# Kernel optimization log

Hardware: AMD Instinct MI355X
Metric: run time of the kernel (lower is better)

## Reference

```python
import jax, jax.numpy as jnp
import numpy as np

NUM_NODES = 200000
NUM_EDGES = 1250000
DIM = 64
K_LAYERS = 3
BATCH = 4096
CAND = 101  # 1 positive + 100 negatives


def setup_inputs() -> dict:
    key = jax.random.key(0)
    k1, k2, k3 = jax.random.split(key, 3)
    emb = jax.random.normal(k1, (NUM_NODES, DIM), dtype=jnp.float32)
    edge_index = jax.random.randint(k2, (2, NUM_EDGES), 0, NUM_NODES)
    batch = jax.random.randint(k3, (BATCH, CAND, 3), 0, NUM_NODES)
    return {"emb": emb, "edge_index": edge_index, "batch": batch,
            "num_nodes": NUM_NODES}


def reference(emb, edge_index, batch, num_nodes):
    # --- LightGCN.get_embedding: K rounds of symmetric-normalized SpMM ---
    row, col = edge_index[0], edge_index[1]  # source -> target
    ones = jnp.ones(row.shape[0], dtype=emb.dtype)
    deg = jax.ops.segment_sum(ones, col, num_segments=num_nodes)  # in-degree
    deg_safe = jnp.where(deg > 0, deg, 1.0)
    dis = jnp.where(deg > 0, jax.lax.rsqrt(deg_safe), 0.0)  # deg^{-1/2}, inf->0
    norm = dis[row] * dis[col]  # [E]

    alpha = 1.0 / (K_LAYERS + 1)  # uniform layer combination
    x = emb
    out = x * alpha
    for _ in range(K_LAYERS):
        # propagate: out[i] = sum_{(j->i)} norm_e * x[j]
        x = jax.ops.segment_sum(x[row] * norm[:, None], col,
                                num_segments=num_nodes)
        out = out + x * alpha

    # --- scoring: gather user/item embeddings, elementwise dot ---
    user_idx = batch[:, :, 0].reshape(-1)
    item_idx = batch[:, :, 1].reshape(-1)
    logits = jnp.sum(out[user_idx] * out[item_idx], axis=-1)  # [B*CAND]
    return logits.reshape(batch.shape[0], -1)
```

## Files before the change

### kernel.cpp

```cpp
#include <hip/hip_runtime.h>

#define DIM 64
#define BSHIFT 8
#define MAXNB 1024
#define CHUNK 4096

__device__ inline unsigned packbf(float a, float b) {
    unsigned ua = __float_as_uint(a), ub = __float_as_uint(b);
    unsigned ra = (ua + 0x7FFFu + ((ua >> 16) & 1u)) >> 16;
    unsigned rb = (ub + 0x7FFFu + ((ub >> 16) & 1u)) >> 16;
    return ra | (rb << 16);
}
__device__ inline void unpackbf(unsigned u, float& lo, float& hi) {
    lo = __uint_as_float(u << 16);
    hi = __uint_as_float(u & 0xFFFF0000u);
}
__device__ inline void acc_row(const uint4 v, float* s) {
    float lo, hi;
    unpackbf(v.x, lo, hi); s[0] += lo; s[1] += hi;
    unpackbf(v.y, lo, hi); s[2] += lo; s[3] += hi;
    unpackbf(v.z, lo, hi); s[4] += lo; s[5] += hi;
    unpackbf(v.w, lo, hi); s[6] += lo; s[7] += hi;
}
__device__ inline void acc_row_m(const uint4 v, float m, float* s) {
    float lo, hi;
    unpackbf(v.x, lo, hi); s[0] = fmaf(m, lo, s[0]); s[1] = fmaf(m, hi, s[1]);
    unpackbf(v.y, lo, hi); s[2] = fmaf(m, lo, s[2]); s[3] = fmaf(m, hi, s[3]);
    unpackbf(v.z, lo, hi); s[4] = fmaf(m, lo, s[4]); s[5] = fmaf(m, hi, s[5]);
    unpackbf(v.w, lo, hi); s[6] = fmaf(m, lo, s[6]); s[7] = fmaf(m, hi, s[7]);
}

__global__ __launch_bounds__(256) void block_hist_kernel(
        const int* __restrict__ col, int* __restrict__ H, int E, int NB,
        int nblocks) {
    __shared__ int h[MAXNB];
    int tid = threadIdx.x;
    for (int k = tid; k < NB; k += 256) h[k] = 0;
    __syncthreads();
    int base = blockIdx.x * CHUNK;
    #pragma unroll
    for (int k = 0; k < CHUNK / 256; k++) {
        int e = base + tid + k * 256;
        if (e < E) atomicAdd(&h[col[e] >> BSHIFT], 1);
    }
    __syncthreads();
    for (int k = tid; k < NB; k += 256) H[(size_t)k * nblocks + blockIdx.x] = h[k];
}

__global__ void scan_tile_sum_kernel(const int* __restrict__ H,
                                     int* __restrict__ T, int M) {
    int tid = threadIdx.x;
    int base = blockIdx.x * 1024 + tid * 4;
    int s = 0;
    #pragma unroll
    for (int k = 0; k < 4; k++)
        if (base + k < M) s += H[base + k];
    __shared__ int lds[256];
    lds[tid] = s;
    __syncthreads();
    for (int off = 128; off > 0; off >>= 1) {
        if (tid < off) lds[tid] += lds[tid + off];
        __syncthreads();
    }
    if (tid == 0) T[blockIdx.x] = lds[0];
}

__global__ void scan_tile_offsets_kernel(int* __restrict__ T, int nt) {
    __shared__ int lds[256];
    int tid = threadIdx.x;
    int v = (tid < nt) ? T[tid] : 0;
    lds[tid] = v;
    __syncthreads();
    for (int off = 1; off < 256; off <<= 1) {
        int t = (tid >= off) ? lds[tid - off] : 0;
        __syncthreads();
        lds[tid] += t;
        __syncthreads();
    }
    if (tid < nt) T[tid] = lds[tid] - v;
}

__global__ void scan_final_kernel(const int* __restrict__ H,
                                  const int* __restrict__ T,
                                  int* __restrict__ S, int M) {
    int tid = threadIdx.x;
    int base = blockIdx.x * 1024 + tid * 4;
    int c[4];
    int local = 0;
    #pragma unroll
    for (int k = 0; k < 4; k++) {
        c[k] = (base + k < M) ? H[base + k] : 0;
        local += c[k];
    }
    __shared__ int lds[256];
    lds[tid] = local;
    __syncthreads();
    for (int off = 1; off < 256; off <<= 1) {
        int t = (tid >= off) ? lds[tid - off] : 0;
        __syncthreads();
        lds[tid] += t;
        __syncthreads();
    }
    int excl = lds[tid] - local + T[blockIdx.x];
    #pragma unroll
    for (int k = 0; k < 4; k++) {
        if (base + k < M) S[base + k] = excl;
        excl += c[k];
    }
}

__global__ void bbase_kernel(const int* __restrict__ S, int* __restrict__ bbase,
                             int NB, int nblocks, int E) {
    int k = blockIdx.x * blockDim.x + threadIdx.x;
    if (k < NB) bbase[k] = S[(size_t)k * nblocks];
    if (k == 0) bbase[NB] = E;
}

__global__ __launch_bounds__(256) void scatter_binned_kernel(
        const int* __restrict__ row, const int* __restrict__ col,
        const int* __restrict__ S, unsigned* __restrict__ pairs, int E,
        int NB, int nblocks) {
    __shared__ unsigned stage[CHUNK];
    __shared__ int gdst[CHUNK];
    __shared__ int hist[MAXNB];
    __shared__ int pfx[MAXNB];
    __shared__ int gbase[MAXNB];
    int tid = threadIdx.x;
    int bid = blockIdx.x;
    int base = bid * CHUNK;
    int nloc = min(CHUNK, E - base);

    for (int b = tid; b < NB; b += 256) hist[b] = 0;
    __syncthreads();

    unsigned vals[CHUNK / 256];
    int keys[CHUNK / 256];
    #pragma unroll
    for (int k = 0; k < CHUNK / 256; k++) {
        int e = base + tid + k * 256;
        if (e < E) {
            int d = col[e];
            int s = row[e];
            keys[k] = d >> BSHIFT;
            vals[k] = (unsigned)s | ((unsigned)(d & 255) << 24);
            atomicAdd(&hist[keys[k]], 1);
        } else {
            keys[k] = -1;
        }
    }
    __syncthreads();

    int b0 = tid * 4;
    int c4[4];
    int loc = 0;
    #pragma unroll
    for (int k = 0; k < 4; k++) {
        c4[k] = (b0 + k < NB) ? hist[b0 + k] : 0;
        loc += c4[k];
    }
    gbase[tid] = loc;
    __syncthreads();
    for (int off = 1; off < 256; off <<= 1) {
        int t = (tid >= off) ? gbase[tid - off] : 0;
        __syncthreads();
        gbase[tid] += t;
        __syncthreads();
    }
    int excl = gbase[tid] - loc;
    #pragma unroll
    for (int k = 0; k < 4; k++) {
        if (b0 + k < NB) pfx[b0 + k] = excl;
        excl += c4[k];
    }
    __syncthreads();

    for (int b = tid; b < NB; b += 256) {
        gbase[b] = S[(size_t)b * nblocks + bid];
        hist[b] = pfx[b];
    }
    __syncthreads();

    #pragma unroll
    for (int k = 0; k < CHUNK / 256; k++) {
        if (keys[k] >= 0) {
            int slot = atomicAdd(&hist[keys[k]], 1);
            stage[slot] = vals[k];
            gdst[slot] = gbase[keys[k]] + (slot - pfx[keys[k]]);
        }
    }
    __syncthreads();

    for (int s = tid; s < nloc; s += 256) pairs[gdst[s]] = stage[s];
}

__global__ void fine_fill_kernel(const unsigned* __restrict__ pairs,
                                 const int* __restrict__ bbase,
                                 int* __restrict__ row_ptr,
                                 int* __restrict__ csr_src, int N, int E) {
    __shared__ int cnt[256];
    __shared__ int cur[256];
    int b = blockIdx.x;
    int tid = threadIdx.x;
    int beg = bbase[b], end = bbase[b + 1];
    cnt[tid] = 0;
    __syncthreads();
    for (int j = beg + tid; j < end; j += 256)
        atomicAdd(&cnt[pairs[j] >> 24], 1);
    __syncthreads();
    int v = cnt[tid];
    for (int off = 1; off < 256; off <<= 1) {
        int t = (tid >= off) ? cnt[tid - off] : 0;
        __syncthreads();
        cnt[tid] += t;
        __syncthreads();
    }
    int excl = cnt[tid] - v;
    int node = (b << BSHIFT) + tid;
    if (node < N) row_ptr[node] = beg + excl;
    cur[tid] = beg + excl;
    __syncthreads();
    for (int j = beg + tid; j < end; j += 256) {
        unsigned p = pairs[j];
        int pos = atomicAdd(&cur[p >> 24], 1);
        csr_src[pos] = (int)(p & 0xFFFFFFu);
    }
    if (b == 0 && tid == 0) row_ptr[N] = E;
}

__global__ void prescale_kernel(const float4* __restrict__ emb4,
                                const int* __restrict__ row_ptr,
                                uint4* __restrict__ z4, int N) {
    int t = blockIdx.x * blockDim.x + threadIdx.x;
    int i = t >> 3;
    int gl = t & 7;
    if (i >= N) return;
    int deg = row_ptr[i + 1] - row_ptr[i];
    float wd = (deg > 0) ? rsqrtf((float)deg) : 0.0f;
    size_t eo = (size_t)i * 16 + gl * 2;
    float4 a = emb4[eo], b = emb4[eo + 1];
    uint4 z;
    z.x = packbf(a.x * wd, a.y * wd);
    z.y = packbf(a.z * wd, a.w * wd);
    z.z = packbf(b.x * wd, b.y * wd);
    z.w = packbf(b.z * wd, b.w * wd);
    z4[(size_t)i * 8 + gl] = z;
}

__device__ inline void row_gather_sum(const int* __restrict__ csr_src,
                                      const uint4* __restrict__ z4, int b,
                                      int e, int gl, float* s) {
    if (b >= e) return;
    int e1 = e - 1;
    int j = b;
    int i0 = csr_src[j];
    int i1 = csr_src[min(j + 1, e1)];
    int i2 = csr_src[min(j + 2, e1)];
    int i3 = csr_src[min(j + 3, e1)];
    while (j < e) {
        uint4 v0 = z4[(size_t)i0 * 8 + gl];
        uint4 v1 = z4[(size_t)i1 * 8 + gl];
        uint4 v2 = z4[(size_t)i2 * 8 + gl];
        uint4 v3 = z4[(size_t)i3 * 8 + gl];
        int jn = j + 4;
        if (jn < e) {
            i0 = csr_src[jn];
            i1 = csr_src[min(jn + 1, e1)];
            i2 = csr_src[min(jn + 2, e1)];
            i3 = csr_src[min(jn + 3, e1)];
        }
        float m1 = (j + 1 < e) ? 1.0f : 0.0f;
        float m2 = (j + 2 < e) ? 1.0f : 0.0f;
        float m3 = (j + 3 < e) ? 1.0f : 0.0f;
        acc_row(v0, s);
        acc_row_m(v1, m1, s);
        acc_row_m(v2, m2, s);
        acc_row_m(v3, m3, s);
        j = jn;
    }
}

__global__ void spmm_pull_kernel(const int* __restrict__ row_ptr,
                                 const int* __restrict__ csr_src,
                                 const uint4* __restrict__ z4,
                                 uint4* __restrict__ znext4, int N) {
    int t = blockIdx.x * blockDim.x + threadIdx.x;
    int i = t >> 3;
    int gl = t & 7;
    if (i >= N) return;
    int b = row_ptr[i], e = row_ptr[i + 1];
    float s[8] = {0, 0, 0, 0, 0, 0, 0, 0};
    row_gather_sum(csr_src, z4, b, e, gl, s);
    int deg = e - b;
    float wd = (deg > 0) ? rsqrtf((float)deg) : 0.0f;
    float w2 = wd * wd;
    uint4 z;
    z.x = packbf(s[0] * w2, s[1] * w2);
    z.y = packbf(s[2] * w2, s[3] * w2);
    z.z = packbf(s[4] * w2, s[5] * w2);
    z.w = packbf(s[6] * w2, s[7] * w2);
    znext4[(size_t)i * 8 + gl] = z;
}

__global__ void spmm_combine_kernel(const int* __restrict__ row_ptr,
                                    const int* __restrict__ csr_src,
                                    const uint4* __restrict__ z2,
                                    const uint4* __restrict__ z1,
                                    const float4* __restrict__ emb4,
                                    uint4* __restrict__ accb, int N) {
    int t = blockIdx.x * blockDim.x + threadIdx.x;
    int i = t >> 3;
    int gl = t & 7;
    if (i >= N) return;
    int b = row_ptr[i], e = row_ptr[i + 1];
    float s[8] = {0, 0, 0, 0, 0, 0, 0, 0};
    row_gather_sum(csr_src, z2, b, e, gl, s);
    int deg = e - b;
    float wd = (deg > 0) ? rsqrtf((float)deg) : 0.0f;
    float sq = (deg > 0) ? sqrtf((float)deg) : 0.0f;
    size_t zo = (size_t)i * 8 + gl;
    uint4 a1 = z1[zo], a2 = z2[zo];
    float w[8] = {0, 0, 0, 0, 0, 0, 0, 0};
    acc_row(a1, w); acc_row(a2, w);
    size_t eo = (size_t)i * 16 + gl * 2;
    float4 e0 = emb4[eo], e1 = emb4[eo + 1];
    float r0 = e0.x + sq * w[0] + wd * s[0];
    float r1 = e0.y + sq * w[1] + wd * s[1];
    float r2 = e0.z + sq * w[2] + wd * s[2];
    float r3 = e0.w + sq * w[3] + wd * s[3];
    float r4 = e1.x + sq * w[4] + wd * s[4];
    float r5 = e1.y + sq * w[5] + wd * s[5];
    float r6 = e1.z + sq * w[6] + wd * s[6];
    float r7 = e1.w + sq * w[7] + wd * s[7];
    uint4 z;
    z.x = packbf(r0, r1);
    z.y = packbf(r2, r3);
    z.z = packbf(r4, r5);
    z.w = packbf(r6, r7);
    accb[zo] = z;
}

__global__ void score_kernel(const int* __restrict__ batch,
                             const uint4* __restrict__ accb,
                             float* __restrict__ out, int P) {
    int t = blockIdx.x * blockDim.x + threadIdx.x;
    int p = t >> 3;
    int gl = t & 7;
    if (p >= P) return;
    int u = batch[(size_t)p * 3 + 0];
    int it = batch[(size_t)p * 3 + 1];
    uint4 a = accb[(size_t)u * 8 + gl];
    uint4 b = accb[(size_t)it * 8 + gl];
    float sa[8] = {0, 0, 0, 0, 0, 0, 0, 0};
    float sb[8] = {0, 0, 0, 0, 0, 0, 0, 0};
    acc_row(a, sa);
    acc_row(b, sb);
    float s = sa[0] * sb[0] + sa[1] * sb[1] + sa[2] * sb[2] + sa[3] * sb[3] +
              sa[4] * sb[4] + sa[5] * sb[5] + sa[6] * sb[6] + sa[7] * sb[7];
    s += __shfl_xor(s, 4, 64);
    s += __shfl_xor(s, 2, 64);
    s += __shfl_xor(s, 1, 64);
    if (gl == 0) out[p] = s * 0.0625f;
}

extern "C" void kernel_launch(void* const* d_in, const int* in_sizes, int n_in,
                              void* d_out, int out_size, void* d_ws,
                              size_t ws_size, hipStream_t stream) {
    const float* emb = (const float*)d_in[0];
    const int* edge_index = (const int*)d_in[1];
    const int* batch = (const int*)d_in[2];
    float* out = (float*)d_out;

    const int N = in_sizes[0] / DIM;
    const int E = in_sizes[1] / 2;
    const int P = out_size;
    const int NB = (N + 255) >> BSHIFT;
    const int nblocks = (E + CHUNK - 1) / CHUNK;
    const int M = NB * nblocks;
    const int nt = (M + 1023) / 1024;

    const int* row = edge_index;
    const int* col = edge_index + E;

    const size_t zbytes = (size_t)N * DIM * 2;

    auto align256 = [](size_t x) { return (x + 255) & ~(size_t)255; };
    char* ws = (char*)d_ws;
    uint4* z0   = (uint4*)ws; ws += align256(zbytes);
    uint4* z1   = (uint4*)ws; ws += align256(zbytes);
    uint4* z2   = (uint4*)ws; ws += align256(zbytes);
    uint4* accb = (uint4*)ws; ws += align256(zbytes);
    unsigned* pairs = (unsigned*)ws; ws += align256((size_t)E * 4);
    int* csr_src    = (int*)ws;      ws += align256((size_t)E * 4);
    int* row_ptr    = (int*)ws;      ws += align256((size_t)(N + 1) * 4);
    int* H          = (int*)ws;      ws += align256((size_t)M * 4);
    int* S          = (int*)ws;      ws += align256((size_t)M * 4);
    int* T          = (int*)ws;      ws += align256(256 * 4);
    int* bbase      = (int*)ws;

    block_hist_kernel<<<nblocks, 256, 0, stream>>>(col, H, E, NB, nblocks);
    scan_tile_sum_kernel<<<nt, 256, 0, stream>>>(H, T, M);
    scan_tile_offsets_kernel<<<1, 256, 0, stream>>>(T, nt);
    scan_final_kernel<<<nt, 256, 0, stream>>>(H, T, S, M);
    bbase_kernel<<<(NB + 255) / 256, 256, 0, stream>>>(S, bbase, NB, nblocks, E);
    scatter_binned_kernel<<<nblocks, 256, 0, stream>>>(row, col, S, pairs, E,
                                                       NB, nblocks);
    fine_fill_kernel<<<NB, 256, 0, stream>>>(pairs, bbase, row_ptr, csr_src,
                                             N, E);

    const int nodeBlocks = (N * 8 + 255) / 256;

    prescale_kernel<<<nodeBlocks, 256, 0, stream>>>((const float4*)emb,
                                                    row_ptr, z0, N);

    spmm_pull_kernel<<<nodeBlocks, 256, 0, stream>>>(row_ptr, csr_src, z0, z1, N);
    spmm_pull_kernel<<<nodeBlocks, 256, 0, stream>>>(row_ptr, csr_src, z1, z2, N);
    spmm_combine_kernel<<<nodeBlocks, 256, 0, stream>>>(row_ptr, csr_src, z2,
                                                        z1, (const float4*)emb,
                                                        accb, N);

    score_kernel<<<(P * 8 + 255) / 256, 256, 0, stream>>>(batch, accb, out, P);
}
```

Measured before the change: 249.9 us.

## Fuse bbase into scan, cache bf16 emb, use wave-sized blocks, two pairs per score group

```diff
diff --git a/kernel.cpp b/kernel.cpp
--- a/kernel.cpp
+++ b/kernel.cpp
@@ -82,7 +82,9 @@
 
 __global__ void scan_final_kernel(const int* __restrict__ H,
                                   const int* __restrict__ T,
-                                  int* __restrict__ S, int M) {
+                                  int* __restrict__ S,
+                                  int* __restrict__ bbase, int M, int nblocks,
+                                  int NB, int E) {
     int tid = threadIdx.x;
     int base = blockIdx.x * 1024 + tid * 4;
     int c[4];
@@ -104,16 +106,14 @@
     int excl = lds[tid] - local + T[blockIdx.x];
     #pragma unroll
     for (int k = 0; k < 4; k++) {
-        if (base + k < M) S[base + k] = excl;
+        int m = base + k;
+        if (m < M) {
+            S[m] = excl;
+            if (m % nblocks == 0) bbase[m / nblocks] = excl;
+        }
         excl += c[k];
     }
-}
-
-__global__ void bbase_kernel(const int* __restrict__ S, int* __restrict__ bbase,
-                             int NB, int nblocks, int E) {
-    int k = blockIdx.x * blockDim.x + threadIdx.x;
-    if (k < NB) bbase[k] = S[(size_t)k * nblocks];
-    if (k == 0) bbase[NB] = E;
+    if (blockIdx.x == 0 && tid == 0) bbase[NB] = E;
 }
 
 __global__ __launch_bounds__(256) void scatter_binned_kernel(
@@ -229,7 +229,8 @@
 
 __global__ void prescale_kernel(const float4* __restrict__ emb4,
                                 const int* __restrict__ row_ptr,
-                                uint4* __restrict__ z4, int N) {
+                                uint4* __restrict__ z4,
+                                uint4* __restrict__ embb, int N) {
     int t = blockIdx.x * blockDim.x + threadIdx.x;
     int i = t >> 3;
     int gl = t & 7;
@@ -238,12 +239,19 @@
     float wd = (deg > 0) ? rsqrtf((float)deg) : 0.0f;
     size_t eo = (size_t)i * 16 + gl * 2;
     float4 a = emb4[eo], b = emb4[eo + 1];
+    size_t zo = (size_t)i * 8 + gl;
+    uint4 eb;
+    eb.x = packbf(a.x, a.y);
+    eb.y = packbf(a.z, a.w);
+    eb.z = packbf(b.x, b.y);
+    eb.w = packbf(b.z, b.w);
+    embb[zo] = eb;
     uint4 z;
     z.x = packbf(a.x * wd, a.y * wd);
     z.y = packbf(a.z * wd, a.w * wd);
     z.z = packbf(b.x * wd, b.y * wd);
     z.w = packbf(b.z * wd, b.w * wd);
-    z4[(size_t)i * 8 + gl] = z;
+    z4[zo] = z;
 }
 
 __device__ inline void row_gather_sum(const int* __restrict__ csr_src,
@@ -279,11 +287,10 @@
     }
 }
 
-__global__ void spmm_pull_kernel(const int* __restrict__ row_ptr,
-                                 const int* __restrict__ csr_src,
-                                 const uint4* __restrict__ z4,
-                                 uint4* __restrict__ znext4, int N) {
-    int t = blockIdx.x * blockDim.x + threadIdx.x;
+__global__ __launch_bounds__(64) void spmm_pull_kernel(
+        const int* __restrict__ row_ptr, const int* __restrict__ csr_src,
+        const uint4* __restrict__ z4, uint4* __restrict__ znext4, int N) {
+    int t = blockIdx.x * 64 + threadIdx.x;
     int i = t >> 3;
     int gl = t & 7;
     if (i >= N) return;
@@ -301,13 +308,11 @@
     znext4[(size_t)i * 8 + gl] = z;
 }
 
-__global__ void spmm_combine_kernel(const int* __restrict__ row_ptr,
-                                    const int* __restrict__ csr_src,
-                                    const uint4* __restrict__ z2,
-                                    const uint4* __restrict__ z1,
-                                    const float4* __restrict__ emb4,
-                                    uint4* __restrict__ accb, int N) {
-    int t = blockIdx.x * blockDim.x + threadIdx.x;
+__global__ __launch_bounds__(64) void spmm_combine_kernel(
+        const int* __restrict__ row_ptr, const int* __restrict__ csr_src,
+        const uint4* __restrict__ z2, const uint4* __restrict__ z1,
+        const uint4* __restrict__ embb, uint4* __restrict__ accb, int N) {
+    int t = blockIdx.x * 64 + threadIdx.x;
     int i = t >> 3;
     int gl = t & 7;
     if (i >= N) return;
@@ -321,45 +326,60 @@
     uint4 a1 = z1[zo], a2 = z2[zo];
     float w[8] = {0, 0, 0, 0, 0, 0, 0, 0};
     acc_row(a1, w); acc_row(a2, w);
-    size_t eo = (size_t)i * 16 + gl * 2;
-    float4 e0 = emb4[eo], e1 = emb4[eo + 1];
-    float r0 = e0.x + sq * w[0] + wd * s[0];
-    float r1 = e0.y + sq * w[1] + wd * s[1];
-    float r2 = e0.z + sq * w[2] + wd * s[2];
-    float r3 = e0.w + sq * w[3] + wd * s[3];
-    float r4 = e1.x + sq * w[4] + wd * s[4];
-    float r5 = e1.y + sq * w[5] + wd * s[5];
-    float r6 = e1.z + sq * w[6] + wd * s[6];
-    float r7 = e1.w + sq * w[7] + wd * s[7];
+    uint4 eb = embb[zo];
+    float em[8] = {0, 0, 0, 0, 0, 0, 0, 0};
+    acc_row(eb, em);
+    float r[8];
+    #pragma unroll
+    for (int k = 0; k < 8; k++) r[k] = em[k] + sq * w[k] + wd * s[k];
     uint4 z;
-    z.x = packbf(r0, r1);
-    z.y = packbf(r2, r3);
-    z.z = packbf(r4, r5);
-    z.w = packbf(r6, r7);
+    z.x = packbf(r[0], r[1]);
+    z.y = packbf(r[2], r[3]);
+    z.z = packbf(r[4], r[5]);
+    z.w = packbf(r[6], r[7]);
     accb[zo] = z;
 }
 
-__global__ void score_kernel(const int* __restrict__ batch,
-                             const uint4* __restrict__ accb,
-                             float* __restrict__ out, int P) {
-    int t = blockIdx.x * blockDim.x + threadIdx.x;
-    int p = t >> 3;
+__global__ __launch_bounds__(64) void score_kernel(
+        const int* __restrict__ batch, const uint4* __restrict__ accb,
+        float* __restrict__ out, int P) {
+    int t = blockIdx.x * 64 + threadIdx.x;
+    int g = t >> 3;
     int gl = t & 7;
-    if (p >= P) return;
-    int u = batch[(size_t)p * 3 + 0];
-    int it = batch[(size_t)p * 3 + 1];
-    uint4 a = accb[(size_t)u * 8 + gl];
-    uint4 b = accb[(size_t)it * 8 + gl];
-    float sa[8] = {0, 0, 0, 0, 0, 0, 0, 0};
-    float sb[8] = {0, 0, 0, 0, 0, 0, 0, 0};
-    acc_row(a, sa);
-    acc_row(b, sb);
-    float s = sa[0] * sb[0] + sa[1] * sb[1] + sa[2] * sb[2] + sa[3] * sb[3] +
-              sa[4] * sb[4] + sa[5] * sb[5] + sa[6] * sb[6] + sa[7] * sb[7];
-    s += __shfl_xor(s, 4, 64);
-    s += __shfl_xor(s, 2, 64);
-    s += __shfl_xor(s, 1, 64);
-    if (gl == 0) out[p] = s * 0.0625f;
+    int p0 = g * 2;
+    if (p0 >= P) return;
+    int p1 = min(p0 + 1, P - 1);
+    int u0 = batch[(size_t)p0 * 3 + 0];
+    int i0 = batch[(size_t)p0 * 3 + 1];
+    int u1 = batch[(size_t)p1 * 3 + 0];
+    int i1 = batch[(size_t)p1 * 3 + 1];
+    uint4 a0 = accb[(size_t)u0 * 8 + gl];
+    uint4 b0 = accb[(size_t)i0 * 8 + gl];
+    uint4 a1 = accb[(size_t)u1 * 8 + gl];
+    uint4 b1 = accb[(size_t)i1 * 8 + gl];
+    float sa[8], sb[8];
+    #pragma unroll
+    for (int k = 0; k < 8; k++) { sa[k] = 0; sb[k] = 0; }
+    acc_row(a0, sa);
+    acc_row(b0, sb);
+    float s0 = sa[0] * sb[0] + sa[1] * sb[1] + sa[2] * sb[2] + sa[3] * sb[3] +
+               sa[4] * sb[4] + sa[5] * sb[5] + sa[6] * sb[6] + sa[7] * sb[7];
+    #pragma unroll
+    for (int k = 0; k < 8; k++) { sa[k] = 0; sb[k] = 0; }
+    acc_row(a1, sa);
+    acc_row(b1, sb);
+    float s1 = sa[0] * sb[0] + sa[1] * sb[1] + sa[2] * sb[2] + sa[3] * sb[3] +
+               sa[4] * sb[4] + sa[5] * sb[5] + sa[6] * sb[6] + sa[7] * sb[7];
+    s0 += __shfl_xor(s0, 4, 64);
+    s0 += __shfl_xor(s0, 2, 64);
+    s0 += __shfl_xor(s0, 1, 64);
+    s1 += __shfl_xor(s1, 4, 64);
+    s1 += __shfl_xor(s1, 2, 64);
+    s1 += __shfl_xor(s1, 1, 64);
+    if (gl == 0) {
+        out[p0] = s0 * 0.0625f;
+        if (p0 + 1 < P) out[p0 + 1] = s1 * 0.0625f;
+    }
 }
 
 extern "C" void kernel_launch(void* const* d_in, const int* in_sizes, int n_in,
@@ -389,6 +409,7 @@
     uint4* z1   = (uint4*)ws; ws += align256(zbytes);
     uint4* z2   = (uint4*)ws; ws += align256(zbytes);
     uint4* accb = (uint4*)ws; ws += align256(zbytes);
+    uint4* embb = (uint4*)ws; ws += align256(zbytes);
     unsigned* pairs = (unsigned*)ws; ws += align256((size_t)E * 4);
     int* csr_src    = (int*)ws;      ws += align256((size_t)E * 4);
     int* row_ptr    = (int*)ws;      ws += align256((size_t)(N + 1) * 4);
@@ -400,23 +421,22 @@
     block_hist_kernel<<<nblocks, 256, 0, stream>>>(col, H, E, NB, nblocks);
     scan_tile_sum_kernel<<<nt, 256, 0, stream>>>(H, T, M);
     scan_tile_offsets_kernel<<<1, 256, 0, stream>>>(T, nt);
-    scan_final_kernel<<<nt, 256, 0, stream>>>(H, T, S, M);
-    bbase_kernel<<<(NB + 255) / 256, 256, 0, stream>>>(S, bbase, NB, nblocks, E);
+    scan_final_kernel<<<nt, 256, 0, stream>>>(H, T, S, bbase, M, nblocks, NB, E);
     scatter_binned_kernel<<<nblocks, 256, 0, stream>>>(row, col, S, pairs, E,
                                                        NB, nblocks);
     fine_fill_kernel<<<NB, 256, 0, stream>>>(pairs, bbase, row_ptr, csr_src,
                                              N, E);
 
-    const int nodeBlocks = (N * 8 + 255) / 256;
-
-    prescale_kernel<<<nodeBlocks, 256, 0, stream>>>((const float4*)emb,
-                                                    row_ptr, z0, N);
-
-    spmm_pull_kernel<<<nodeBlocks, 256, 0, stream>>>(row_ptr, csr_src, z0, z1, N);
-    spmm_pull_kernel<<<nodeBlocks, 256, 0, stream>>>(row_ptr, csr_src, z1, z2, N);
-    spmm_combine_kernel<<<nodeBlocks, 256, 0, stream>>>(row_ptr, csr_src, z2,
-                                                        z1, (const float4*)emb,
-                                                        accb, N);
-
-    score_kernel<<<(P * 8 + 255) / 256, 256, 0, stream>>>(batch, accb, out, P);
-}
+    const int nodeBlocks256 = (N * 8 + 255) / 256;
+    prescale_kernel<<<nodeBlocks256, 256, 0, stream>>>((const float4*)emb,
+                                                       row_ptr, z0, embb, N);
+
+    const int waveBlocks = (N + 7) / 8;
+    spmm_pull_kernel<<<waveBlocks, 64, 0, stream>>>(row_ptr, csr_src, z0, z1, N);
+    spmm_pull_kernel<<<waveBlocks, 64, 0, stream>>>(row_ptr, csr_src, z1, z2, N);
+    spmm_combine_kernel<<<waveBlocks, 64, 0, stream>>>(row_ptr, csr_src, z2,
+                                                       z1, embb, accb, N);
+
+    const int scoreBlocks = (P + 15) / 16;
+    score_kernel<<<scoreBlocks, 64, 0, stream>>>(batch, accb, out, P);
+}
```

After: 257.4 us. +3.0%, slower.
